# Performance work log

Hardware: AMD Instinct MI355X
Metric: run time of the kernel (lower is better)

Reference implementation:

```python
import jax, jax.numpy as jnp
import numpy as np

N_NODES = 50000
N_EDGES = 800000
IN_F = 128
HEADS = 8
D_HEAD = 16  # out_features // num_heads = 128 // 8


def setup_inputs() -> dict:
    key = jax.random.key(0)
    k1, k2, k3, k4, k5 = jax.random.split(key, 5)
    x = jax.random.normal(k1, (N_NODES, IN_F), dtype=jnp.float32)
    edge_index = jax.random.randint(k2, (2, N_EDGES), 0, N_NODES, dtype=jnp.int64)
    # nn.Linear weight is [out, in]; xavier-ish scale
    W = jax.random.normal(k3, (HEADS * D_HEAD, IN_F), dtype=jnp.float32) * (1.0 / np.sqrt(IN_F))
    a_src = jax.random.normal(k4, (HEADS, D_HEAD), dtype=jnp.float32) * (1.0 / np.sqrt(D_HEAD))
    a_dst = jax.random.normal(k5, (HEADS, D_HEAD), dtype=jnp.float32) * (1.0 / np.sqrt(D_HEAD))
    return {"x": x, "edge_index": edge_index, "W": W, "a_src": a_src, "a_dst": a_dst}


def reference(x, edge_index, W, a_src, a_dst):
    N = x.shape[0]
    H, D = a_src.shape
    # h = W x, reshaped to [N, H, D]
    h = (x @ W.T).reshape(N, H, D)
    src, dst = edge_index[0], edge_index[1]
    # per-node attention logits, then gather per-edge (same math as gathering h first)
    s_src = jnp.einsum("nhd,hd->nh", h, a_src)  # [N, H]
    s_dst = jnp.einsum("nhd,hd->nh", h, a_dst)  # [N, H]
    attn = jax.nn.leaky_relu(s_src[src] + s_dst[dst], negative_slope=0.2)  # [E, H]
    # torch scatter_reduce amax onto a zeros tensor -> max is clamped at 0
    attn_max = jnp.maximum(jax.ops.segment_max(attn, dst, num_segments=N), 0.0)  # [N, H]
    e = jnp.exp(attn - attn_max[dst])  # [E, H]
    attn_sum = jax.ops.segment_sum(e, dst, num_segments=N)  # [N, H]
    alpha = e / (attn_sum[dst] + 1e-10)  # [E, H] (dropout is identity in eval)
    msg = h[src] * alpha[..., None]  # [E, H, D]
    out = jax.ops.segment_sum(msg, dst, num_segments=N)  # [N, H, D]
    return out.reshape(N, H * D)
```

## Files before the change

kernel.cpp:

```cpp
#include <hip/hip_runtime.h>
#include <hip/hip_bf16.h>

#define N_NODES 50000
#define N_EDGES 800000
#define HEADS 8
#define MAXDEG 64
#define NPB 4
#define NPART 8
#define PART_SZ 6250
#define CHUNK_EDGES 2048
#define NCHUNK ((N_EDGES + CHUNK_EDGES - 1) / CHUNK_EDGES)

using frag_ab = __attribute__((ext_vector_type(8))) short;
using frag_cd = __attribute__((ext_vector_type(4))) float;

static __device__ __forceinline__ short f2bs(float v) {
    __hip_bfloat16 b = __float2bfloat16(v);
    return *(short*)&b;
}

__global__ __launch_bounds__(256) void k_wc(const float* __restrict__ W,
                                            const float* __restrict__ a_src,
                                            const float* __restrict__ a_dst,
                                            __hip_bfloat16* __restrict__ Wcb,
                                            int* __restrict__ cursor) {
    int tid = blockIdx.x * 256 + threadIdx.x;
    for (int i = tid; i < N_NODES; i += gridDim.x * 256) cursor[i] = 0;
    if (tid >= 144 * 128) return;
    int r = tid >> 7, k = tid & 127;
    float v;
    if (r < 128) {
        v = W[tid];
    } else {
        int hd = (r - 128) & 7;
        const float* av = (r < 136) ? a_src : a_dst;
        v = 0.f;
        #pragma unroll
        for (int d = 0; d < 16; ++d)
            v += av[hd * 16 + d] * W[(size_t)(hd * 16 + d) * 128 + k];
    }
    Wcb[tid] = __float2bfloat16(v);
}

__global__ __launch_bounds__(256) void k_fill(const int* __restrict__ ei,
                                              int* __restrict__ cursor,
                                              int* __restrict__ csr_ell) {
    const int part = blockIdx.x & (NPART - 1);
    const int chunk = blockIdx.x >> 3;
    const int lo = part * PART_SZ;
    const int e0 = chunk * CHUNK_EDGES;
    const int t = threadIdx.x;

    #pragma unroll
    for (int half = 0; half < 2; ++half) {
        int base = e0 + half * 1024 + t * 4;
        if (base >= N_EDGES) continue;
        int4 d4 = *(const int4*)(ei + N_EDGES + base);
        int4 s4 = *(const int4*)(ei + base);
        int dd[4] = { d4.x, d4.y, d4.z, d4.w };
        int ss[4] = { s4.x, s4.y, s4.z, s4.w };
        #pragma unroll
        for (int u = 0; u < 4; ++u) {
            unsigned rel = (unsigned)(dd[u] - lo);
            if (rel < PART_SZ) {
                int pos = atomicAdd(&cursor[dd[u]], 1);
                if (pos < MAXDEG) csr_ell[dd[u] * MAXDEG + pos] = ss[u];
            }
        }
    }
}

__global__ __launch_bounds__(256) void k_mfma(const float* __restrict__ x,
                                              const __hip_bfloat16* __restrict__ Wcb,
                                              __hip_bfloat16* __restrict__ hb,
                                              float* __restrict__ s_src,
                                              float* __restrict__ s_dst) {
    __shared__ short Ws[144][136];
    const int t = threadIdx.x;
    for (int i = t; i < 144 * 16; i += 256) {
        int r = i >> 4, c = (i & 15) << 3;
        frag_ab v = *(const frag_ab*)((const short*)Wcb + (size_t)r * 128 + c);
        *(frag_ab*)&Ws[r][c] = v;
    }
    __syncthreads();

    const int wave = t >> 6, lane = t & 63;
    const int rb0 = blockIdx.x * 128 + wave * 16;
    if (rb0 >= N_NODES) return;
    const int rb1 = rb0 + 64;
    const int m16 = lane & 15, kg = lane >> 4;
    const int arow0 = min(rb0 + m16, N_NODES - 1);
    const int arow1 = min(rb1 + m16, N_NODES - 1);
    const float* ab0 = x + (size_t)arow0 * 128 + kg * 8;
    const float* ab1 = x + (size_t)arow1 * 128 + kg * 8;

    frag_cd acc[2][9];
    #pragma unroll
    for (int r = 0; r < 2; ++r)
        #pragma unroll
        for (int j = 0; j < 9; ++j) acc[r][j] = (frag_cd){0.f, 0.f, 0.f, 0.f};

    #pragma unroll
    for (int ks = 0; ks < 4; ++ks) {
        float4 p0 = *(const float4*)(ab0 + ks * 32);
        float4 p1 = *(const float4*)(ab0 + ks * 32 + 4);
        float4 q0 = *(const float4*)(ab1 + ks * 32);
        float4 q1 = *(const float4*)(ab1 + ks * 32 + 4);
        frag_ab af0, af1;
        af0[0] = f2bs(p0.x); af0[1] = f2bs(p0.y); af0[2] = f2bs(p0.z); af0[3] = f2bs(p0.w);
        af0[4] = f2bs(p1.x); af0[5] = f2bs(p1.y); af0[6] = f2bs(p1.z); af0[7] = f2bs(p1.w);
        af1[0] = f2bs(q0.x); af1[1] = f2bs(q0.y); af1[2] = f2bs(q0.z); af1[3] = f2bs(q0.w);
        af1[4] = f2bs(q1.x); af1[5] = f2bs(q1.y); af1[6] = f2bs(q1.z); af1[7] = f2bs(q1.w);
        #pragma unroll
        for (int nt = 0; nt < 9; ++nt) {
            frag_ab bf = *(const frag_ab*)&Ws[nt * 16 + m16][ks * 32 + kg * 8];
            acc[0][nt] = __builtin_amdgcn_mfma_f32_16x16x32_bf16(af0, bf, acc[0][nt], 0, 0, 0);
            acc[1][nt] = __builtin_amdgcn_mfma_f32_16x16x32_bf16(af1, bf, acc[1][nt], 0, 0, 0);
        }
    }

    #pragma unroll
    for (int r = 0; r < 2; ++r) {
        int rbase = r ? rb1 : rb0;
        #pragma unroll
        for (int nt = 0; nt < 9; ++nt) {
            #pragma unroll
            for (int j = 0; j < 4; ++j) {
                int row = rbase + kg * 4 + j;
                if (row >= N_NODES) continue;
                int col = nt * 16 + m16;
                float v = acc[r][nt][j];
                if (col < 128)      hb[(size_t)row * 128 + col] = __float2bfloat16(v);
                else if (col < 136) s_src[row * 8 + (col - 128)] = v;
                else                s_dst[row * 8 + (col - 136)] = v;
            }
        }
    }
}

__global__ __launch_bounds__(256) void k_gather(const int* __restrict__ csr_ell,
                                                const int* __restrict__ cursor,
                                                const float* __restrict__ s_src,
                                                const float* __restrict__ s_dst,
                                                const __hip_bfloat16* __restrict__ hb,
                                                float* __restrict__ out) {
    __shared__ int   csr_l[NPB][MAXDEG];
    __shared__ float sa[NPB][MAXDEG][9];
    const int slot = threadIdx.x >> 6;
    const int lane = threadIdx.x & 63;
    const int n = blockIdx.x * NPB + slot;
    if (n >= N_NODES) return;
    const int hd8 = lane >> 3, l8 = lane & 7;
    const int deg = min(cursor[n], MAXDEG);
    const float sdst = s_dst[n * 8 + hd8];

    if (lane < deg) csr_l[slot][lane] = csr_ell[n * MAXDEG + lane];

    float m = 0.f;
    for (int j = l8; j < deg; j += 8) {
        float a = s_src[csr_l[slot][j] * 8 + hd8] + sdst;
        a = a > 0.f ? a : 0.2f * a;
        sa[slot][j][hd8] = a;
        m = fmaxf(m, a);
    }
    #pragma unroll
    for (int mask = 1; mask <= 4; mask <<= 1)
        m = fmaxf(m, __shfl_xor(m, mask));

    float s = 0.f;
    for (int j = l8; j < deg; j += 8) {
        float w = __expf(sa[slot][j][hd8] - m);
        sa[slot][j][hd8] = w;
        s += w;
    }
    #pragma unroll
    for (int mask = 1; mask <= 4; mask <<= 1)
        s += __shfl_xor(s, mask);
    float rcp = 1.0f / (s + 1e-10f);

    const int half = lane >> 5;
    const int fl = lane & 31;
    const int hd2 = fl >> 2;
    const float rcp2 = __shfl(rcp, hd2 * 8);

    const unsigned short* hbs = (const unsigned short*)hb;
    float4 acc = {0.f, 0.f, 0.f, 0.f};
    int j = 0;
    for (; j + 8 <= deg; j += 8) {
        #pragma unroll
        for (int u = 0; u < 4; ++u) {
            int jj = j + 2 * u + half;
            int src = csr_l[slot][jj];
            float w = sa[slot][jj][hd2];
            uint2 v = *(const uint2*)(hbs + (size_t)src * 128 + fl * 4);
            acc.x += w * __uint_as_float(v.x << 16);
            acc.y += w * __uint_as_float(v.x & 0xffff0000u);
            acc.z += w * __uint_as_float(v.y << 16);
            acc.w += w * __uint_as_float(v.y & 0xffff0000u);
        }
    }
    for (; j + 2 <= deg; j += 2) {
        int jj = j + half;
        int src = csr_l[slot][jj];
        float w = sa[slot][jj][hd2];
        uint2 v = *(const uint2*)(hbs + (size_t)src * 128 + fl * 4);
        acc.x += w * __uint_as_float(v.x << 16);
        acc.y += w * __uint_as_float(v.x & 0xffff0000u);
        acc.z += w * __uint_as_float(v.y << 16);
        acc.w += w * __uint_as_float(v.y & 0xffff0000u);
    }
    if (j < deg && half == 0) {
        int src = csr_l[slot][j];
        float w = sa[slot][j][hd2];
        uint2 v = *(const uint2*)(hbs + (size_t)src * 128 + fl * 4);
        acc.x += w * __uint_as_float(v.x << 16);
        acc.y += w * __uint_as_float(v.x & 0xffff0000u);
        acc.z += w * __uint_as_float(v.y << 16);
        acc.w += w * __uint_as_float(v.y & 0xffff0000u);
    }

    acc.x += __shfl_xor(acc.x, 32);
    acc.y += __shfl_xor(acc.y, 32);
    acc.z += __shfl_xor(acc.z, 32);
    acc.w += __shfl_xor(acc.w, 32);
    if (half == 0) {
        float4 o = { acc.x * rcp2, acc.y * rcp2, acc.z * rcp2, acc.w * rcp2 };
        *(float4*)(out + (size_t)n * 128 + fl * 4) = o;
    }
}

extern "C" void kernel_launch(void* const* d_in, const int* in_sizes, int n_in,
                              void* d_out, int out_size, void* d_ws, size_t ws_size,
                              hipStream_t stream) {
    const float* x     = (const float*)d_in[0];
    const int*   ei    = (const int*)d_in[1];
    const float* W     = (const float*)d_in[2];
    const float* a_src = (const float*)d_in[3];
    const float* a_dst = (const float*)d_in[4];
    float* out = (float*)d_out;

    char* ws = (char*)d_ws;
    __hip_bfloat16* hb      = (__hip_bfloat16*)(ws);
    __hip_bfloat16* Wcb     = (__hip_bfloat16*)(ws + 12800000);
    float*          s_src   = (float*)(ws + 12840000);
    float*          s_dst   = (float*)(ws + 14440000);
    int*            cursor  = (int*)  (ws + 16040000);
    int*            csr_ell = (int*)  (ws + 16240000);

    k_wc    <<<(144 * 128 + 255) / 256, 256, 0, stream>>>(W, a_src, a_dst, Wcb, cursor);
    k_fill  <<<NCHUNK * NPART, 256, 0, stream>>>(ei, cursor, csr_ell);
    k_mfma  <<<(N_NODES + 127) / 128, 256, 0, stream>>>(x, Wcb, hb, s_src, s_dst);
    k_gather<<<(N_NODES + NPB - 1) / NPB, 256, 0, stream>>>(csr_ell, cursor, s_src, s_dst, hb, out);
}
```

Measured before the change: 101.4 us.

## Fuse CSR fill into MFMA kernel and widen gather loads to 16 bytes

The edge-fill (ELL build) kernel and the MFMA projection kernel now run as one launch, with extra blocks doing the fill, so the two independent stages overlap and one launch is saved. The gather loop also changes its lane mapping: each lane loads 8 bf16 features (uint4) and four edges are processed in parallel per wave, with a 16-edge unrolled loop. This should raise memory-level parallelism in the neighbour gather. The cost is more registers, an extra cross-lane reduction step, and MFMA blocks that allocate shared memory sharing the launch with lightweight fill blocks.

```diff
diff --git a/kernel.cpp b/kernel.cpp
--- a/kernel.cpp
+++ b/kernel.cpp
@@ -10,6 +10,8 @@
 #define PART_SZ 6250
 #define CHUNK_EDGES 2048
 #define NCHUNK ((N_EDGES + CHUNK_EDGES - 1) / CHUNK_EDGES)
+#define NMFMA ((N_NODES + 127) / 128)
+#define NFILLB (NCHUNK * NPART)
 
 using frag_ab = __attribute__((ext_vector_type(8))) short;
 using frag_cd = __attribute__((ext_vector_type(4))) float;
@@ -42,41 +44,44 @@
     Wcb[tid] = __float2bfloat16(v);
 }
 
-__global__ __launch_bounds__(256) void k_fill(const int* __restrict__ ei,
-                                              int* __restrict__ cursor,
-                                              int* __restrict__ csr_ell) {
-    const int part = blockIdx.x & (NPART - 1);
-    const int chunk = blockIdx.x >> 3;
-    const int lo = part * PART_SZ;
-    const int e0 = chunk * CHUNK_EDGES;
-    const int t = threadIdx.x;
-
-    #pragma unroll
-    for (int half = 0; half < 2; ++half) {
-        int base = e0 + half * 1024 + t * 4;
-        if (base >= N_EDGES) continue;
-        int4 d4 = *(const int4*)(ei + N_EDGES + base);
-        int4 s4 = *(const int4*)(ei + base);
-        int dd[4] = { d4.x, d4.y, d4.z, d4.w };
-        int ss[4] = { s4.x, s4.y, s4.z, s4.w };
-        #pragma unroll
-        for (int u = 0; u < 4; ++u) {
-            unsigned rel = (unsigned)(dd[u] - lo);
-            if (rel < PART_SZ) {
-                int pos = atomicAdd(&cursor[dd[u]], 1);
-                if (pos < MAXDEG) csr_ell[dd[u] * MAXDEG + pos] = ss[u];
-            }
-        }
-    }
-}
-
-__global__ __launch_bounds__(256) void k_mfma(const float* __restrict__ x,
-                                              const __hip_bfloat16* __restrict__ Wcb,
-                                              __hip_bfloat16* __restrict__ hb,
-                                              float* __restrict__ s_src,
-                                              float* __restrict__ s_dst) {
+__global__ __launch_bounds__(256) void k_fm(const float* __restrict__ x,
+                                            const __hip_bfloat16* __restrict__ Wcb,
+                                            __hip_bfloat16* __restrict__ hb,
+                                            float* __restrict__ s_src,
+                                            float* __restrict__ s_dst,
+                                            const int* __restrict__ ei,
+                                            int* __restrict__ cursor,
+                                            int* __restrict__ csr_ell) {
     __shared__ short Ws[144][136];
     const int t = threadIdx.x;
+
+    if (blockIdx.x >= NMFMA) {
+        const int fb = blockIdx.x - NMFMA;
+        const int part = fb & (NPART - 1);
+        const int chunk = fb >> 3;
+        const int lo = part * PART_SZ;
+        const int e0 = chunk * CHUNK_EDGES;
+
+        #pragma unroll
+        for (int half = 0; half < 2; ++half) {
+            int base = e0 + half * 1024 + t * 4;
+            if (base >= N_EDGES) continue;
+            int4 d4 = *(const int4*)(ei + N_EDGES + base);
+            int4 s4 = *(const int4*)(ei + base);
+            int dd[4] = { d4.x, d4.y, d4.z, d4.w };
+            int ss[4] = { s4.x, s4.y, s4.z, s4.w };
+            #pragma unroll
+            for (int u = 0; u < 4; ++u) {
+                unsigned rel = (unsigned)(dd[u] - lo);
+                if (rel < PART_SZ) {
+                    int pos = atomicAdd(&cursor[dd[u]], 1);
+                    if (pos < MAXDEG) csr_ell[dd[u] * MAXDEG + pos] = ss[u];
+                }
+            }
+        }
+        return;
+    }
+
     for (int i = t; i < 144 * 16; i += 256) {
         int r = i >> 4, c = (i & 15) << 3;
         frag_ab v = *(const frag_ab*)((const short*)Wcb + (size_t)r * 128 + c);
@@ -178,54 +183,64 @@
         s += __shfl_xor(s, mask);
     float rcp = 1.0f / (s + 1e-10f);
 
-    const int half = lane >> 5;
-    const int fl = lane & 31;
-    const int hd2 = fl >> 2;
-    const float rcp2 = __shfl(rcp, hd2 * 8);
+    const int q = lane >> 4;
+    const int fl = lane & 15;
+    const int hd = fl >> 1;
+    const float rcpq = __shfl(rcp, hd * 8);
 
     const unsigned short* hbs = (const unsigned short*)hb;
-    float4 acc = {0.f, 0.f, 0.f, 0.f};
+    float acc[8] = {0.f, 0.f, 0.f, 0.f, 0.f, 0.f, 0.f, 0.f};
+
     int j = 0;
-    for (; j + 8 <= deg; j += 8) {
-        #pragma unroll
-        for (int u = 0; u < 4; ++u) {
-            int jj = j + 2 * u + half;
+    for (; j + 16 <= deg; j += 16) {
+        int  jj0 = j + q,      jj1 = j + 4 + q,  jj2 = j + 8 + q,  jj3 = j + 12 + q;
+        int  s0 = csr_l[slot][jj0], s1 = csr_l[slot][jj1];
+        int  s2 = csr_l[slot][jj2], s3 = csr_l[slot][jj3];
+        float w0 = sa[slot][jj0][hd], w1 = sa[slot][jj1][hd];
+        float w2 = sa[slot][jj2][hd], w3 = sa[slot][jj3][hd];
+        uint4 v0 = *(const uint4*)(hbs + (size_t)s0 * 128 + fl * 8);
+        uint4 v1 = *(const uint4*)(hbs + (size_t)s1 * 128 + fl * 8);
+        uint4 v2 = *(const uint4*)(hbs + (size_t)s2 * 128 + fl * 8);
+        uint4 v3 = *(const uint4*)(hbs + (size_t)s3 * 128 + fl * 8);
+        #define ACC8(vv, ww) \
+            acc[0] += (ww) * __uint_as_float((vv).x << 16); \
+            acc[1] += (ww) * __uint_as_float((vv).x & 0xffff0000u); \
+            acc[2] += (ww) * __uint_as_float((vv).y << 16); \
+            acc[3] += (ww) * __uint_as_float((vv).y & 0xffff0000u); \
+            acc[4] += (ww) * __uint_as_float((vv).z << 16); \
+            acc[5] += (ww) * __uint_as_float((vv).z & 0xffff0000u); \
+            acc[6] += (ww) * __uint_as_float((vv).w << 16); \
+            acc[7] += (ww) * __uint_as_float((vv).w & 0xffff0000u);
+        ACC8(v0, w0) ACC8(v1, w1) ACC8(v2, w2) ACC8(v3, w3)
+    }
+    for (; j + 4 <= deg; j += 4) {
+        int jj = j + q;
+        int src = csr_l[slot][jj];
+        float w = sa[slot][jj][hd];
+        uint4 v = *(const uint4*)(hbs + (size_t)src * 128 + fl * 8);
+        ACC8(v, w)
+    }
+    if (j < deg) {
+        int jj = j + q;
+        if (jj < deg) {
             int src = csr_l[slot][jj];
-            float w = sa[slot][jj][hd2];
-            uint2 v = *(const uint2*)(hbs + (size_t)src * 128 + fl * 4);
-            acc.x += w * __uint_as_float(v.x << 16);
-            acc.y += w * __uint_as_float(v.x & 0xffff0000u);
-            acc.z += w * __uint_as_float(v.y << 16);
-            acc.w += w * __uint_as_float(v.y & 0xffff0000u);
-        }
-    }
-    for (; j + 2 <= deg; j += 2) {
-        int jj = j + half;
-        int src = csr_l[slot][jj];
-        float w = sa[slot][jj][hd2];
-        uint2 v = *(const uint2*)(hbs + (size_t)src * 128 + fl * 4);
-        acc.x += w * __uint_as_float(v.x << 16);
-        acc.y += w * __uint_as_float(v.x & 0xffff0000u);
-        acc.z += w * __uint_as_float(v.y << 16);
-        acc.w += w * __uint_as_float(v.y & 0xffff0000u);
-    }
-    if (j < deg && half == 0) {
-        int src = csr_l[slot][j];
-        float w = sa[slot][j][hd2];
-        uint2 v = *(const uint2*)(hbs + (size_t)src * 128 + fl * 4);
-        acc.x += w * __uint_as_float(v.x << 16);
-        acc.y += w * __uint_as_float(v.x & 0xffff0000u);
-        acc.z += w * __uint_as_float(v.y << 16);
-        acc.w += w * __uint_as_float(v.y & 0xffff0000u);
-    }
-
-    acc.x += __shfl_xor(acc.x, 32);
-    acc.y += __shfl_xor(acc.y, 32);
-    acc.z += __shfl_xor(acc.z, 32);
-    acc.w += __shfl_xor(acc.w, 32);
-    if (half == 0) {
-        float4 o = { acc.x * rcp2, acc.y * rcp2, acc.z * rcp2, acc.w * rcp2 };
-        *(float4*)(out + (size_t)n * 128 + fl * 4) = o;
+            float w = sa[slot][jj][hd];
+            uint4 v = *(const uint4*)(hbs + (size_t)src * 128 + fl * 8);
+            ACC8(v, w)
+        }
+    }
+    #undef ACC8
+
+    #pragma unroll
+    for (int k = 0; k < 8; ++k) {
+        acc[k] += __shfl_xor(acc[k], 16);
+        acc[k] += __shfl_xor(acc[k], 32);
+    }
+    if (q == 0) {
+        float4 o0 = { acc[0] * rcpq, acc[1] * rcpq, acc[2] * rcpq, acc[3] * rcpq };
+        float4 o1 = { acc[4] * rcpq, acc[5] * rcpq, acc[6] * rcpq, acc[7] * rcpq };
+        *(float4*)(out + (size_t)n * 128 + fl * 8)     = o0;
+        *(float4*)(out + (size_t)n * 128 + fl * 8 + 4) = o1;
     }
 }
 
@@ -248,7 +263,6 @@
     int*            csr_ell = (int*)  (ws + 16240000);
 
     k_wc    <<<(144 * 128 + 255) / 256, 256, 0, stream>>>(W, a_src, a_dst, Wcb, cursor);
-    k_fill  <<<NCHUNK * NPART, 256, 0, stream>>>(ei, cursor, csr_ell);
-    k_mfma  <<<(N_NODES + 127) / 128, 256, 0, stream>>>(x, Wcb, hb, s_src, s_dst);
+    k_fm    <<<NMFMA + NFILLB, 256, 0, stream>>>(x, Wcb, hb, s_src, s_dst, ei, cursor, csr_ell);
     k_gather<<<(N_NODES + NPB - 1) / NPB, 256, 0, stream>>>(csr_ell, cursor, s_src, s_dst, hb, out);
 }
```

New measurement: 91.19 us. 1.11x faster.
